# Optimization experiments

Hardware: AMD Instinct MI355X
Metric: run time of the kernel (lower is better)

Reference implementation:

```python
import jax, jax.numpy as jnp
import numpy as np

B, G, IN, H, OUT = 4096, 8, 512, 1024, 64


def setup_inputs() -> dict:
    key = jax.random.key(0)
    k0, k1, k2, k3 = jax.random.split(key, 4)
    x = jax.random.normal(k0, (B, IN), dtype=jnp.float32)
    gid = jax.random.randint(k1, (B,), 0, G, dtype=jnp.int32)
    # Per-group 2-layer MLP params (Kaiming-ish scaling)
    W1 = jax.random.normal(k2, (G, IN, H), dtype=jnp.float32) / np.sqrt(IN)
    b1 = jnp.zeros((G, H), dtype=jnp.float32)
    W2 = jax.random.normal(k3, (G, H, OUT), dtype=jnp.float32) / np.sqrt(H)
    b2 = jnp.zeros((G, OUT), dtype=jnp.float32)
    return {"x": x, "gid": gid, "W1": W1, "b1": b1, "W2": W2, "b2": b2}


def reference(x, gid, W1, b1, W2, b2):
    # Routed 2-layer MLP: each sample i uses expert head gid[i].
    # Compute all G group GEMMs (grouped-GEMM style), then select the
    # routed row per sample with a one-hot contraction (no [B,IN,H]
    # per-sample weight materialization).
    onehot = jax.nn.one_hot(gid, W1.shape[0], dtype=x.dtype)  # [B, G]
    h_all = jnp.einsum('bi,gih->bgh', x, W1) + b1[None]       # [B, G, H]
    h = jax.nn.relu(jnp.einsum('bgh,bg->bh', h_all, onehot))  # [B, H]
    y_all = jnp.einsum('bh,gho->bgo', h, W2) + b2[None]       # [B, G, OUT]
    y = jnp.einsum('bgo,bg->bo', y_all, onehot)               # [B, OUT]
    return y
```

## Files before the change

kernel.cpp:

```cpp
#include <hip/hip_runtime.h>
#include <hip/hip_bf16.h>

#define B_ 4096
#define G_ 8
#define IN_ 512
#define H_ 1024
#define OUT_ 64
#define MAXT 72

typedef float f32x4 __attribute__((ext_vector_type(4)));
typedef __bf16 bf16x8 __attribute__((ext_vector_type(8)));
typedef unsigned short u16x8 __attribute__((ext_vector_type(8)));

__device__ inline unsigned short f2bf(float f) {
  unsigned int u = __builtin_bit_cast(unsigned int, f);
  u += 0x7fffu + ((u >> 16) & 1u);
  return (unsigned short)(u >> 16);
}

__device__ inline u16x8 pack8(float4 a, float4 b) {
  return u16x8{f2bf(a.x), f2bf(a.y), f2bf(a.z), f2bf(a.w),
               f2bf(b.x), f2bf(b.y), f2bf(b.z), f2bf(b.w)};
}

__device__ inline bool tile_lookup(const int* __restrict__ meta, int mt,
                                   int& g, int& row0, int& start, int& cnt) {
  int ts = 0;
  bool found = false;
#pragma unroll
  for (int gg = 0; gg < G_; gg++) {
    int s = meta[gg], e = meta[gg + 1];
    int T = (e - s + 63) >> 6;
    if (!found && mt >= ts && mt < ts + T) {
      g = gg;
      row0 = (mt - ts) << 6;
      start = s;
      cnt = e - s;
      found = true;
    }
    ts += T;
  }
  return found;
}

__global__ __launch_bounds__(256) void transpose_w1_kernel(
    const float* __restrict__ W1, unsigned short* __restrict__ W1t) {
  __shared__ float tile[32][33];
  int b = blockIdx.x;
  int h32 = b & 31, k32 = (b >> 5) & 15, g = b >> 9;
  int t = threadIdx.x;
  int kl = t >> 3, nl = (t & 7) * 4;
  const float* src =
      W1 + ((size_t)g * IN_ + k32 * 32 + kl) * H_ + h32 * 32 + nl;
  float4 v = *(const float4*)src;
  tile[kl][nl + 0] = v.x;
  tile[kl][nl + 1] = v.y;
  tile[kl][nl + 2] = v.z;
  tile[kl][nl + 3] = v.w;
  __syncthreads();
  int nl2 = t >> 3, kl2 = (t & 7) * 4;
  ushort4 o;
  o.x = f2bf(tile[kl2 + 0][nl2]);
  o.y = f2bf(tile[kl2 + 1][nl2]);
  o.z = f2bf(tile[kl2 + 2][nl2]);
  o.w = f2bf(tile[kl2 + 3][nl2]);
  *(ushort4*)(W1t + ((size_t)g * H_ + h32 * 32 + nl2) * IN_ + k32 * 32 +
              kl2) = o;
}

__global__ __launch_bounds__(256) void bucket_kernel(
    const int* __restrict__ gid, int* __restrict__ meta,
    int* __restrict__ perm) {
  __shared__ unsigned short lc[256][G_];
  __shared__ int offs_s[G_ + 1];
  int t = threadIdx.x;
#pragma unroll
  for (int g = 0; g < G_; g++) lc[t][g] = 0;
  int myg[16];
  const int base = t * 16;
#pragma unroll
  for (int j = 0; j < 16; j++) {
    myg[j] = gid[base + j];
    lc[t][myg[j]]++;
  }
  __syncthreads();
  if (t < G_) {
    int run = 0;
    for (int tt = 0; tt < 256; tt++) {
      int v = lc[tt][t];
      lc[tt][t] = (unsigned short)run;
      run += v;
    }
    offs_s[t + 1] = run;
  }
  __syncthreads();
  if (t == 0) {
    int o = 0;
    for (int g = 0; g < G_; g++) {
      int c = offs_s[g + 1];
      offs_s[g] = o;
      meta[g] = o;
      o += c;
    }
    offs_s[G_] = o;
    meta[G_] = o;
  }
  __syncthreads();
  int cur[G_];
#pragma unroll
  for (int g = 0; g < G_; g++) cur[g] = offs_s[g] + (int)lc[t][g];
#pragma unroll
  for (int j = 0; j < 16; j++) {
    int g = myg[j];
    perm[cur[g]++] = base + j;
  }
}

__global__ __launch_bounds__(256) void gemm1_kernel(
    const float* __restrict__ x, const unsigned short* __restrict__ W1t,
    const float* __restrict__ b1, const int* __restrict__ meta,
    const int* __restrict__ perm, unsigned short* __restrict__ hb) {
  int b = blockIdx.x;
  int mt = b >> 4, nt = b & 15;
  int g, row0, start, cnt;
  if (!tile_lookup(meta, mt, g, row0, start, cnt)) return;
  int n0 = nt * 64;

  __shared__ __attribute__((aligned(16))) unsigned short As[64 * 64];
  __shared__ __attribute__((aligned(16))) unsigned short Bs[64 * 64];
  __shared__ int rows[64];

  int tid = threadIdx.x;
  int lane = tid & 63;
  int wv = tid >> 6;

  if (tid < 64) rows[tid] = perm[start + min(row0 + tid, cnt - 1)];
  __syncthreads();

  int r = tid >> 2, c4 = tid & 3;
  const float* xsrc = x + (size_t)rows[r] * IN_ + c4 * 16;
  unsigned short* adst0 = &As[r * 64 + (((2 * c4) ^ (r & 7)) << 3)];
  unsigned short* adst1 = &As[r * 64 + (((2 * c4 + 1) ^ (r & 7)) << 3)];

  int brow0 = wv * 16 + (lane >> 3);
  int brow1 = brow0 + 8;
  int bsl = lane & 7;
  const unsigned short* bsrc0 = W1t + ((size_t)g * H_ + n0 + brow0) * IN_ +
                                ((bsl ^ (brow0 & 7)) << 3);
  const unsigned short* bsrc1 = W1t + ((size_t)g * H_ + n0 + brow1) * IN_ +
                                ((bsl ^ (brow1 & 7)) << 3);
  unsigned short* bdst0 = &Bs[wv * 1024 + lane * 8];
  unsigned short* bdst1 = &Bs[wv * 1024 + 512 + lane * 8];

  int fl = lane & 15, q = lane >> 4;
  int m0 = (wv >> 1) * 32, nw = (wv & 1) * 32;
  const unsigned short* apA = &As[(m0 + fl) * 64];
  const unsigned short* apB = &As[(m0 + 16 + fl) * 64];
  const unsigned short* bpA = &Bs[(nw + fl) * 64];
  const unsigned short* bpB = &Bs[(nw + 16 + fl) * 64];

  f32x4 acc[2][2];
#pragma unroll
  for (int i = 0; i < 2; i++)
#pragma unroll
    for (int j = 0; j < 2; j++) acc[i][j] = f32x4{0.f, 0.f, 0.f, 0.f};

  float4 v0 = *(const float4*)(xsrc + 0);
  float4 v1 = *(const float4*)(xsrc + 4);
  float4 v2 = *(const float4*)(xsrc + 8);
  float4 v3 = *(const float4*)(xsrc + 12);

  for (int it = 0; it < 8; it++) {
    int k0 = it * 64;
    u16x8 p0 = pack8(v0, v1);
    u16x8 p1 = pack8(v2, v3);
    u16x8 bw0 = *(const u16x8*)(bsrc0 + k0);
    u16x8 bw1 = *(const u16x8*)(bsrc1 + k0);
    __syncthreads();
    *(u16x8*)adst0 = p0;
    *(u16x8*)adst1 = p1;
    *(u16x8*)bdst0 = bw0;
    *(u16x8*)bdst1 = bw1;
    __syncthreads();
    if (it < 7) {
      int kn = k0 + 64;
      v0 = *(const float4*)(xsrc + kn);
      v1 = *(const float4*)(xsrc + kn + 4);
      v2 = *(const float4*)(xsrc + kn + 8);
      v3 = *(const float4*)(xsrc + kn + 12);
    }
#pragma unroll
    for (int s = 0; s < 2; s++) {
      int off = (((s << 2) + q) ^ (fl & 7)) << 3;
      bf16x8 a0 = *(const bf16x8*)(apA + off);
      bf16x8 a1 = *(const bf16x8*)(apB + off);
      bf16x8 fb0 = *(const bf16x8*)(bpA + off);
      bf16x8 fb1 = *(const bf16x8*)(bpB + off);
      acc[0][0] = __builtin_amdgcn_mfma_f32_16x16x32_bf16(a0, fb0, acc[0][0], 0, 0, 0);
      acc[1][0] = __builtin_amdgcn_mfma_f32_16x16x32_bf16(a1, fb0, acc[1][0], 0, 0, 0);
      acc[0][1] = __builtin_amdgcn_mfma_f32_16x16x32_bf16(a0, fb1, acc[0][1], 0, 0, 0);
      acc[1][1] = __builtin_amdgcn_mfma_f32_16x16x32_bf16(a1, fb1, acc[1][1], 0, 0, 0);
    }
  }

#pragma unroll
  for (int ni = 0; ni < 2; ni++) {
    int col = n0 + nw + ni * 16 + fl;
    float bias = b1[g * H_ + col];
#pragma unroll
    for (int mi = 0; mi < 2; mi++) {
#pragma unroll
      for (int rg = 0; rg < 4; rg++) {
        int rl = m0 + mi * 16 + q * 4 + rg;
        if (row0 + rl < cnt) {
          float v = fmaxf(acc[mi][ni][rg] + bias, 0.f);
          hb[(size_t)(start + row0 + rl) * H_ + col] = f2bf(v);
        }
      }
    }
  }
}

__global__ __launch_bounds__(256) void gemm2_kernel(
    const unsigned short* __restrict__ hb, const float* __restrict__ W2,
    const float* __restrict__ b2, const int* __restrict__ meta,
    const int* __restrict__ perm, float* __restrict__ y) {
  int mt = blockIdx.x;
  int g, row0, start, cnt;
  if (!tile_lookup(meta, mt, g, row0, start, cnt)) return;

  __shared__ __attribute__((aligned(16))) unsigned short As2[64 * 128];
  __shared__ __attribute__((aligned(16))) unsigned short Bs2[64 * 128];
  __shared__ int rows[64];

  int tid = threadIdx.x;
  int lane = tid & 63;
  int wv = tid >> 6;

  if (tid < 64) rows[tid] = perm[start + min(row0 + tid, cnt - 1)];

  int arow_in_op = lane >> 4;
  int asl = lane & 15;
  int arow[4];
  const unsigned short* asrc[4];
#pragma unroll
  for (int j = 0; j < 4; j++) {
    arow[j] = wv * 16 + j * 4 + arow_in_op;
    int cs = asl ^ (arow[j] & 7);
    asrc[j] = hb + (size_t)(start + min(row0 + arow[j], cnt - 1)) * H_ +
              (cs << 3);
  }

  int kk = tid >> 1;
  int nh = (tid & 1) * 32;
  int kc8 = kk >> 3, kw = kk & 7;

  int fl = lane & 15, q = lane >> 4;
  int m0 = (wv >> 1) * 32, nw = (wv & 1) * 32;
  const unsigned short* apA = &As2[(m0 + fl) * 128];
  const unsigned short* apB = &As2[(m0 + 16 + fl) * 128];
  const unsigned short* bpA = &Bs2[(nw + fl) * 128];
  const unsigned short* bpB = &Bs2[(nw + 16 + fl) * 128];

  f32x4 acc[2][2];
#pragma unroll
  for (int i = 0; i < 2; i++)
#pragma unroll
    for (int j = 0; j < 2; j++) acc[i][j] = f32x4{0.f, 0.f, 0.f, 0.f};

  for (int it = 0; it < 8; it++) {
    int kbase = it * 128;
    u16x8 av[4];
#pragma unroll
    for (int j = 0; j < 4; j++) av[j] = *(const u16x8*)(asrc[j] + kbase);
    const float* wsrc = W2 + ((size_t)g * H_ + kbase + kk) * OUT_ + nh;
    unsigned short bv[32];
#pragma unroll
    for (int i = 0; i < 4; i++) {
      float4 wa = *(const float4*)(wsrc + i * 8);
      float4 wb = *(const float4*)(wsrc + i * 8 + 4);
      bv[i * 8 + 0] = f2bf(wa.x);
      bv[i * 8 + 1] = f2bf(wa.y);
      bv[i * 8 + 2] = f2bf(wa.z);
      bv[i * 8 + 3] = f2bf(wa.w);
      bv[i * 8 + 4] = f2bf(wb.x);
      bv[i * 8 + 5] = f2bf(wb.y);
      bv[i * 8 + 6] = f2bf(wb.z);
      bv[i * 8 + 7] = f2bf(wb.w);
    }
    __syncthreads();
#pragma unroll
    for (int j = 0; j < 4; j++)
      *(u16x8*)&As2[(wv * 16 + j * 4) * 128 + lane * 8] = av[j];
#pragma unroll
    for (int i = 0; i < 32; i++) {
      int n = nh + i;
      Bs2[n * 128 + ((kc8 ^ (n & 7)) << 3) + kw] = bv[i];
    }
    __syncthreads();
#pragma unroll
    for (int s = 0; s < 4; s++) {
      int off = (((s << 2) + q) ^ (fl & 7)) << 3;
      bf16x8 a0 = *(const bf16x8*)(apA + off);
      bf16x8 a1 = *(const bf16x8*)(apB + off);
      bf16x8 fb0 = *(const bf16x8*)(bpA + off);
      bf16x8 fb1 = *(const bf16x8*)(bpB + off);
      acc[0][0] = __builtin_amdgcn_mfma_f32_16x16x32_bf16(a0, fb0, acc[0][0], 0, 0, 0);
      acc[1][0] = __builtin_amdgcn_mfma_f32_16x16x32_bf16(a1, fb0, acc[1][0], 0, 0, 0);
      acc[0][1] = __builtin_amdgcn_mfma_f32_16x16x32_bf16(a0, fb1, acc[0][1], 0, 0, 0);
      acc[1][1] = __builtin_amdgcn_mfma_f32_16x16x32_bf16(a1, fb1, acc[1][1], 0, 0, 0);
    }
  }

#pragma unroll
  for (int ni = 0; ni < 2; ni++) {
    int col = nw + ni * 16 + fl;
    float bias = b2[g * OUT_ + col];
#pragma unroll
    for (int mi = 0; mi < 2; mi++) {
#pragma unroll
      for (int rg = 0; rg < 4; rg++) {
        int rl = m0 + mi * 16 + q * 4 + rg;
        if (row0 + rl < cnt) {
          y[(size_t)rows[rl] * OUT_ + col] = acc[mi][ni][rg] + bias;
        }
      }
    }
  }
}

extern "C" void kernel_launch(void* const* d_in, const int* in_sizes, int n_in,
                              void* d_out, int out_size, void* d_ws,
                              size_t ws_size, hipStream_t stream) {
  const float* x = (const float*)d_in[0];
  const int* gid = (const int*)d_in[1];
  const float* W1 = (const float*)d_in[2];
  const float* b1 = (const float*)d_in[3];
  const float* W2 = (const float*)d_in[4];
  const float* b2 = (const float*)d_in[5];
  float* y = (float*)d_out;

  int* meta = (int*)d_ws;
  int* perm = (int*)((char*)d_ws + 64);
  unsigned short* W1t = (unsigned short*)((char*)d_ws + 16448);
  unsigned short* hb = (unsigned short*)((char*)d_ws + 8405056);

  transpose_w1_kernel<<<4096, 256, 0, stream>>>(W1, W1t);
  bucket_kernel<<<1, 256, 0, stream>>>(gid, meta, perm);
  gemm1_kernel<<<MAXT * 16, 256, 0, stream>>>(x, W1t, b1, meta, perm, hb);
  gemm2_kernel<<<MAXT, 256, 0, stream>>>(hb, W2, b2, meta, perm, y);
}
```

Measured before the change: 128.5 us.

## Pre-convert x and W2 to bf16 in a merged prep kernel

Merges the W1 transpose with a new W2 transpose-to-bf16 and an x-to-bf16 conversion in a single prep launch. gemm1 then loads bf16 x directly instead of converting fp32 per tile, which it previously repeated across all 16 column blocks. gemm2 loads pre-transposed bf16 W2 with vector stores into shared memory instead of 32 scalar scattered stores per thread. The cost is an extra conversion pass over x and W2 and more workspace.

```diff
diff --git a/kernel.cpp b/kernel.cpp
--- a/kernel.cpp
+++ b/kernel.cpp
@@ -43,29 +43,60 @@
   return found;
 }
 
-__global__ __launch_bounds__(256) void transpose_w1_kernel(
-    const float* __restrict__ W1, unsigned short* __restrict__ W1t) {
-  __shared__ float tile[32][33];
+__global__ __launch_bounds__(256) void prep_kernel(
+    const float* __restrict__ W1, const float* __restrict__ W2,
+    const float* __restrict__ x, unsigned short* __restrict__ W1t,
+    unsigned short* __restrict__ W2t, unsigned short* __restrict__ xb) {
   int b = blockIdx.x;
-  int h32 = b & 31, k32 = (b >> 5) & 15, g = b >> 9;
   int t = threadIdx.x;
-  int kl = t >> 3, nl = (t & 7) * 4;
-  const float* src =
-      W1 + ((size_t)g * IN_ + k32 * 32 + kl) * H_ + h32 * 32 + nl;
-  float4 v = *(const float4*)src;
-  tile[kl][nl + 0] = v.x;
-  tile[kl][nl + 1] = v.y;
-  tile[kl][nl + 2] = v.z;
-  tile[kl][nl + 3] = v.w;
-  __syncthreads();
-  int nl2 = t >> 3, kl2 = (t & 7) * 4;
-  ushort4 o;
-  o.x = f2bf(tile[kl2 + 0][nl2]);
-  o.y = f2bf(tile[kl2 + 1][nl2]);
-  o.z = f2bf(tile[kl2 + 2][nl2]);
-  o.w = f2bf(tile[kl2 + 3][nl2]);
-  *(ushort4*)(W1t + ((size_t)g * H_ + h32 * 32 + nl2) * IN_ + k32 * 32 +
-              kl2) = o;
+  if (b < 4096) {
+    __shared__ float tile[32][33];
+    int h32 = b & 31, k32 = (b >> 5) & 15, g = b >> 9;
+    int kl = t >> 3, nl = (t & 7) * 4;
+    const float* src =
+        W1 + ((size_t)g * IN_ + k32 * 32 + kl) * H_ + h32 * 32 + nl;
+    float4 v = *(const float4*)src;
+    tile[kl][nl + 0] = v.x;
+    tile[kl][nl + 1] = v.y;
+    tile[kl][nl + 2] = v.z;
+    tile[kl][nl + 3] = v.w;
+    __syncthreads();
+    int nl2 = t >> 3, kl2 = (t & 7) * 4;
+    ushort4 o;
+    o.x = f2bf(tile[kl2 + 0][nl2]);
+    o.y = f2bf(tile[kl2 + 1][nl2]);
+    o.z = f2bf(tile[kl2 + 2][nl2]);
+    o.w = f2bf(tile[kl2 + 3][nl2]);
+    *(ushort4*)(W1t + ((size_t)g * H_ + h32 * 32 + nl2) * IN_ + k32 * 32 +
+                kl2) = o;
+  } else if (b < 4608) {
+    __shared__ float tile2[32][33];
+    int bb = b - 4096;
+    int g = bb >> 6, k32 = (bb >> 1) & 31, n32 = bb & 1;
+    int kl = t >> 3, nl = (t & 7) * 4;
+    const float* src =
+        W2 + ((size_t)g * H_ + k32 * 32 + kl) * OUT_ + n32 * 32 + nl;
+    float4 v = *(const float4*)src;
+    tile2[kl][nl + 0] = v.x;
+    tile2[kl][nl + 1] = v.y;
+    tile2[kl][nl + 2] = v.z;
+    tile2[kl][nl + 3] = v.w;
+    __syncthreads();
+    int nl2 = t >> 3, kl2 = (t & 7) * 4;
+    ushort4 o;
+    o.x = f2bf(tile2[kl2 + 0][nl2]);
+    o.y = f2bf(tile2[kl2 + 1][nl2]);
+    o.z = f2bf(tile2[kl2 + 2][nl2]);
+    o.w = f2bf(tile2[kl2 + 3][nl2]);
+    *(ushort4*)(W2t + ((size_t)g * OUT_ + n32 * 32 + nl2) * H_ + k32 * 32 +
+                kl2) = o;
+  } else {
+    int bb = b - 4608;
+    size_t base = (size_t)bb * 2048 + t * 8;
+    float4 v0 = *(const float4*)(x + base);
+    float4 v1 = *(const float4*)(x + base + 4);
+    *(u16x8*)(xb + base) = pack8(v0, v1);
+  }
 }
 
 __global__ __launch_bounds__(256) void bucket_kernel(
@@ -117,7 +148,7 @@
 }
 
 __global__ __launch_bounds__(256) void gemm1_kernel(
-    const float* __restrict__ x, const unsigned short* __restrict__ W1t,
+    const unsigned short* __restrict__ xb, const unsigned short* __restrict__ W1t,
     const float* __restrict__ b1, const int* __restrict__ meta,
     const int* __restrict__ perm, unsigned short* __restrict__ hb) {
   int b = blockIdx.x;
@@ -138,7 +169,7 @@
   __syncthreads();
 
   int r = tid >> 2, c4 = tid & 3;
-  const float* xsrc = x + (size_t)rows[r] * IN_ + c4 * 16;
+  const unsigned short* xsrc = xb + (size_t)rows[r] * IN_ + c4 * 16;
   unsigned short* adst0 = &As[r * 64 + (((2 * c4) ^ (r & 7)) << 3)];
   unsigned short* adst1 = &As[r * 64 + (((2 * c4 + 1) ^ (r & 7)) << 3)];
 
@@ -165,29 +196,23 @@
 #pragma unroll
     for (int j = 0; j < 2; j++) acc[i][j] = f32x4{0.f, 0.f, 0.f, 0.f};
 
-  float4 v0 = *(const float4*)(xsrc + 0);
-  float4 v1 = *(const float4*)(xsrc + 4);
-  float4 v2 = *(const float4*)(xsrc + 8);
-  float4 v3 = *(const float4*)(xsrc + 12);
+  u16x8 av0 = *(const u16x8*)(xsrc + 0);
+  u16x8 av1 = *(const u16x8*)(xsrc + 8);
 
   for (int it = 0; it < 8; it++) {
     int k0 = it * 64;
-    u16x8 p0 = pack8(v0, v1);
-    u16x8 p1 = pack8(v2, v3);
     u16x8 bw0 = *(const u16x8*)(bsrc0 + k0);
     u16x8 bw1 = *(const u16x8*)(bsrc1 + k0);
     __syncthreads();
-    *(u16x8*)adst0 = p0;
-    *(u16x8*)adst1 = p1;
+    *(u16x8*)adst0 = av0;
+    *(u16x8*)adst1 = av1;
     *(u16x8*)bdst0 = bw0;
     *(u16x8*)bdst1 = bw1;
     __syncthreads();
     if (it < 7) {
       int kn = k0 + 64;
-      v0 = *(const float4*)(xsrc + kn);
-      v1 = *(const float4*)(xsrc + kn + 4);
-      v2 = *(const float4*)(xsrc + kn + 8);
-      v3 = *(const float4*)(xsrc + kn + 12);
+      av0 = *(const u16x8*)(xsrc + kn);
+      av1 = *(const u16x8*)(xsrc + kn + 8);
     }
 #pragma unroll
     for (int s = 0; s < 2; s++) {
@@ -222,7 +247,7 @@
 }
 
 __global__ __launch_bounds__(256) void gemm2_kernel(
-    const unsigned short* __restrict__ hb, const float* __restrict__ W2,
+    const unsigned short* __restrict__ hb, const unsigned short* __restrict__ W2t,
     const float* __restrict__ b2, const int* __restrict__ meta,
     const int* __restrict__ perm, float* __restrict__ y) {
   int mt = blockIdx.x;
@@ -241,19 +266,23 @@
 
   int arow_in_op = lane >> 4;
   int asl = lane & 15;
-  int arow[4];
   const unsigned short* asrc[4];
 #pragma unroll
   for (int j = 0; j < 4; j++) {
-    arow[j] = wv * 16 + j * 4 + arow_in_op;
-    int cs = asl ^ (arow[j] & 7);
-    asrc[j] = hb + (size_t)(start + min(row0 + arow[j], cnt - 1)) * H_ +
+    int row = wv * 16 + j * 4 + arow_in_op;
+    int cs = asl ^ (row & 7);
+    asrc[j] = hb + (size_t)(start + min(row0 + row, cnt - 1)) * H_ +
               (cs << 3);
   }
 
-  int kk = tid >> 1;
-  int nh = (tid & 1) * 32;
-  int kc8 = kk >> 3, kw = kk & 7;
+  int bn = tid >> 2, qd = tid & 3;
+  const unsigned short* bsrc = W2t + ((size_t)g * OUT_ + bn) * H_ + qd * 32;
+  unsigned short* bdst[4];
+#pragma unroll
+  for (int j = 0; j < 4; j++) {
+    int ch = 4 * qd + j;
+    bdst[j] = &Bs2[bn * 128 + (((ch ^ (bn & 7)) & 15) << 3)];
+  }
 
   int fl = lane & 15, q = lane >> 4;
   int m0 = (wv >> 1) * 32, nw = (wv & 1) * 32;
@@ -273,30 +302,15 @@
     u16x8 av[4];
 #pragma unroll
     for (int j = 0; j < 4; j++) av[j] = *(const u16x8*)(asrc[j] + kbase);
-    const float* wsrc = W2 + ((size_t)g * H_ + kbase + kk) * OUT_ + nh;
-    unsigned short bv[32];
-#pragma unroll
-    for (int i = 0; i < 4; i++) {
-      float4 wa = *(const float4*)(wsrc + i * 8);
-      float4 wb = *(const float4*)(wsrc + i * 8 + 4);
-      bv[i * 8 + 0] = f2bf(wa.x);
-      bv[i * 8 + 1] = f2bf(wa.y);
-      bv[i * 8 + 2] = f2bf(wa.z);
-      bv[i * 8 + 3] = f2bf(wa.w);
-      bv[i * 8 + 4] = f2bf(wb.x);
-      bv[i * 8 + 5] = f2bf(wb.y);
-      bv[i * 8 + 6] = f2bf(wb.z);
-      bv[i * 8 + 7] = f2bf(wb.w);
-    }
+    u16x8 bv[4];
+#pragma unroll
+    for (int j = 0; j < 4; j++) bv[j] = *(const u16x8*)(bsrc + kbase + j * 8);
     __syncthreads();
 #pragma unroll
     for (int j = 0; j < 4; j++)
       *(u16x8*)&As2[(wv * 16 + j * 4) * 128 + lane * 8] = av[j];
 #pragma unroll
-    for (int i = 0; i < 32; i++) {
-      int n = nh + i;
-      Bs2[n * 128 + ((kc8 ^ (n & 7)) << 3) + kw] = bv[i];
-    }
+    for (int j = 0; j < 4; j++) *(u16x8*)bdst[j] = bv[j];
     __syncthreads();
 #pragma unroll
     for (int s = 0; s < 4; s++) {
@@ -342,11 +356,13 @@
 
   int* meta = (int*)d_ws;
   int* perm = (int*)((char*)d_ws + 64);
-  unsigned short* W1t = (unsigned short*)((char*)d_ws + 16448);
-  unsigned short* hb = (unsigned short*)((char*)d_ws + 8405056);
-
-  transpose_w1_kernel<<<4096, 256, 0, stream>>>(W1, W1t);
+  unsigned short* W1t = (unsigned short*)((char*)d_ws + (1u << 16));
+  unsigned short* W2t = (unsigned short*)((char*)d_ws + (16u << 20));
+  unsigned short* xb = (unsigned short*)((char*)d_ws + (24u << 20));
+  unsigned short* hb = (unsigned short*)((char*)d_ws + (32u << 20));
+
+  prep_kernel<<<5632, 256, 0, stream>>>(W1, W2, x, W1t, W2t, xb);
   bucket_kernel<<<1, 256, 0, stream>>>(gid, meta, perm);
-  gemm1_kernel<<<MAXT * 16, 256, 0, stream>>>(x, W1t, b1, meta, perm, hb);
-  gemm2_kernel<<<MAXT, 256, 0, stream>>>(hb, W2, b2, meta, perm, y);
-}
+  gemm1_kernel<<<MAXT * 16, 256, 0, stream>>>(xb, W1t, b1, meta, perm, hb);
+  gemm2_kernel<<<MAXT, 256, 0, stream>>>(hb, W2t, b2, meta, perm, y);
+}
```

Measured after the change: 114.4 us. -11.0%, faster.
